# Kernel optimization log

Hardware: AMD Instinct MI355X
Metric: run time of the kernel (lower is better)

The kernel has to match this reference:

```python
import jax, jax.numpy as jnp
import numpy as np

D_MODEL = 1024
NUM_HEADS = 16
D_K = D_MODEL // NUM_HEADS


def setup_inputs() -> dict:
    key = jax.random.key(0)
    ks = jax.random.split(key, 11)
    B, S = 2, 2048
    s = 1.0 / np.sqrt(D_MODEL)
    return {
        "q": jax.random.normal(ks[0], (B, S, D_MODEL), jnp.float32),
        "k": jax.random.normal(ks[1], (B, S, D_MODEL), jnp.float32),
        "v": jax.random.normal(ks[2], (B, S, D_MODEL), jnp.float32),
        "w_q": jax.random.normal(ks[3], (D_MODEL, D_MODEL), jnp.float32) * s,
        "b_q": jnp.zeros((D_MODEL,), jnp.float32),
        "w_k": jax.random.normal(ks[4], (D_MODEL, D_MODEL), jnp.float32) * s,
        "b_k": jnp.zeros((D_MODEL,), jnp.float32),
        "w_v": jax.random.normal(ks[5], (D_MODEL, D_MODEL), jnp.float32) * s,
        "b_v": jnp.zeros((D_MODEL,), jnp.float32),
        "w_o": jax.random.normal(ks[6], (D_MODEL, D_MODEL), jnp.float32) * s,
        "b_o": jnp.zeros((D_MODEL,), jnp.float32),
    }


def reference(q, k, v, w_q, b_q, w_k, b_k, w_v, b_v, w_o, b_o):
    B, S, _ = q.shape
    H, Dk = NUM_HEADS, D_K

    def split_heads(x):  # [B,S,D] -> [B,H,S,Dk]
        return x.reshape(B, S, H, Dk).transpose(0, 2, 1, 3)

    # torch nn.Linear: x @ W.T + b
    qh = split_heads(q @ w_q.T + b_q)
    kh = split_heads(k @ w_k.T + b_k)
    vh = split_heads(v @ w_v.T + b_v)

    scale = 1.0 / jnp.sqrt(jnp.asarray(Dk, qh.dtype))
    scores = jnp.einsum("bhsd,bhtd->bhst", qh, kh) * scale  # [B,H,S,S]
    attn = jax.nn.softmax(scores, axis=-1)
    # dropout is identity in eval/deterministic baseline
    out = jnp.einsum("bhst,bhtd->bhsd", attn, vh)  # [B,H,S,Dk]
    out = out.transpose(0, 2, 1, 3).reshape(B, S, H * Dk)
    return out @ w_o.T + b_o
```

## Files before the change

kernel.cpp:

```cpp
#include <hip/hip_runtime.h>
#include <hip/hip_bf16.h>
#include <stdint.h>

typedef unsigned short u16;
typedef __attribute__((ext_vector_type(8))) short short8;
typedef __attribute__((ext_vector_type(8))) __bf16 bf16x8;
typedef __attribute__((ext_vector_type(4))) float f32x4;
typedef __attribute__((ext_vector_type(4))) uint32_t u32x4;

#if defined(__has_builtin)
#if __has_builtin(__builtin_amdgcn_global_load_lds)
#define USE_GLLDS 1
#endif
#endif

__device__ __forceinline__ u16 f2bf(float f) {
  __hip_bfloat16 h = __float2bfloat16(f);
  return __builtin_bit_cast(u16, h);
}

__device__ __forceinline__ f32x4 mfma16(bf16x8 a, bf16x8 b, f32x4 c) {
  return __builtin_amdgcn_mfma_f32_16x16x32_bf16(a, b, c, 0, 0, 0);
}

#ifdef USE_GLLDS
__device__ __forceinline__ void async_cp16(const void* g, void* l) {
  __builtin_amdgcn_global_load_lds(
      (const __attribute__((address_space(1))) void*)g,
      (__attribute__((address_space(3))) void*)l, 16, 0, 0);
}
#endif

__global__ __launch_bounds__(256) void cvt_all(
    const float* __restrict__ q, const float* __restrict__ k,
    const float* __restrict__ v, const float* __restrict__ w0,
    const float* __restrict__ w1, const float* __restrict__ w2,
    const float* __restrict__ w3, u16* __restrict__ dst) {
  size_t i = ((size_t)blockIdx.x * 256 + threadIdx.x) * 8;
  const size_t M1 = 1u << 20;
  const float* s;
  size_t base;
  if (i < 4 * M1) { s = q; base = 0; }
  else if (i < 8 * M1) { s = k; base = 4 * M1; }
  else if (i < 12 * M1) { s = v; base = 8 * M1; }
  else if (i < 13 * M1) { s = w0; base = 12 * M1; }
  else if (i < 14 * M1) { s = w1; base = 13 * M1; }
  else if (i < 15 * M1) { s = w2; base = 14 * M1; }
  else { s = w3; base = 15 * M1; }
  const float4 a = *(const float4*)(s + (i - base));
  const float4 b = *(const float4*)(s + (i - base) + 4);
  short8 r;
  r[0] = (short)f2bf(a.x); r[1] = (short)f2bf(a.y);
  r[2] = (short)f2bf(a.z); r[3] = (short)f2bf(a.w);
  r[4] = (short)f2bf(b.x); r[5] = (short)f2bf(b.y);
  r[6] = (short)f2bf(b.z); r[7] = (short)f2bf(b.w);
  *(short8*)(dst + i) = r;
}

__device__ __forceinline__ void gemm_body(const u16* __restrict__ X,
                                          const u16* __restrict__ W,
                                          const float* __restrict__ bias,
                                          void* __restrict__ outp, int mode) {
  __shared__ u16 Al[128 * 64];
  __shared__ u16 Bl[128 * 64];
  const int tid = threadIdx.x;
  const int wv = tid >> 6, l = tid & 63;
  const int wr = wv >> 1, wc = wv & 1;
  const int m0 = blockIdx.y * 128, n0 = blockIdx.x * 128;
  const int lrow = l & 15, lk = (l >> 4) * 8;

  f32x4 acc[4][4];
#pragma unroll
  for (int i = 0; i < 4; ++i)
#pragma unroll
    for (int j = 0; j < 4; ++j) acc[i][j] = (f32x4){0.f, 0.f, 0.f, 0.f};

  const u16* Asrc = X + (size_t)(m0 + (tid >> 3)) * 1024 + (tid & 7) * 8;
  const u16* Bsrc = W + (size_t)(n0 + (tid >> 3)) * 1024 + (tid & 7) * 8;

  for (int kt = 0; kt < 1024; kt += 64) {
#ifdef USE_GLLDS
#pragma unroll
    for (int p = 0; p < 4; ++p) {
      async_cp16(Asrc + (size_t)p * 32 * 1024 + kt, &Al[p * 2048 + wv * 512]);
      async_cp16(Bsrc + (size_t)p * 32 * 1024 + kt, &Bl[p * 2048 + wv * 512]);
    }
#else
    short8 ar[4], br[4];
#pragma unroll
    for (int p = 0; p < 4; ++p) {
      ar[p] = *(const short8*)(Asrc + (size_t)p * 32 * 1024 + kt);
      br[p] = *(const short8*)(Bsrc + (size_t)p * 32 * 1024 + kt);
    }
#pragma unroll
    for (int p = 0; p < 4; ++p) {
      *(short8*)&Al[p * 2048 + tid * 8] = ar[p];
      *(short8*)&Bl[p * 2048 + tid * 8] = br[p];
    }
#endif
    __syncthreads();
#pragma unroll
    for (int ks = 0; ks < 2; ++ks) {
      bf16x8 af[4], bf[4];
#pragma unroll
      for (int mf = 0; mf < 4; ++mf)
        af[mf] = *(const bf16x8*)&Al[(wr * 64 + mf * 16 + lrow) * 64 + ks * 32 + lk];
#pragma unroll
      for (int nf = 0; nf < 4; ++nf)
        bf[nf] = *(const bf16x8*)&Bl[(wc * 64 + nf * 16 + lrow) * 64 + ks * 32 + lk];
#pragma unroll
      for (int mf = 0; mf < 4; ++mf)
#pragma unroll
        for (int nf = 0; nf < 4; ++nf)
          acc[mf][nf] = mfma16(af[mf], bf[nf], acc[mf][nf]);
    }
    __syncthreads();
  }

  const int rb = (l >> 4) * 4;
#pragma unroll
  for (int mf = 0; mf < 4; ++mf) {
#pragma unroll
    for (int nf = 0; nf < 4; ++nf) {
      const int gn = n0 + wc * 64 + nf * 16 + lrow;
      const float bi = bias[gn];
#pragma unroll
      for (int r = 0; r < 4; ++r) {
        const int gm = m0 + wr * 64 + mf * 16 + rb + r;
        float val = acc[mf][nf][r] + bi;
        const int b = gm >> 11, s = gm & 2047, h = gn >> 6, d = gn & 63;
        if (mode == 3) {
          ((float*)outp)[(size_t)gm * 1024 + gn] = val;
        } else if (mode == 2) {
          ((u16*)outp)[(((size_t)((b * 16 + h) * 64 + d)) << 11) + s] = f2bf(val);
        } else {
          if (mode == 0) val *= 0.125f;
          ((u16*)outp)[(((size_t)((b * 16 + h) * 2048 + s)) << 6) + d] = f2bf(val);
        }
      }
    }
  }
}

__global__ __launch_bounds__(256) void gemm_proj(
    const u16* __restrict__ qb, const u16* __restrict__ wqb,
    const float* __restrict__ b_q, const float* __restrict__ b_k,
    const float* __restrict__ b_v, u16* __restrict__ Qh) {
  const int z = blockIdx.z;
  const float* bias = (z == 0) ? b_q : ((z == 1) ? b_k : b_v);
  gemm_body(qb + ((size_t)z << 22), wqb + ((size_t)z << 20), bias,
            Qh + ((size_t)z << 22), z);
}

__global__ __launch_bounds__(256) void gemm_out(
    const u16* __restrict__ X, const u16* __restrict__ W,
    const float* __restrict__ bias, float* __restrict__ out) {
  gemm_body(X, W, bias, out, 3);
}

__global__ __launch_bounds__(512, 4) void flash_attn2(
    const u16* __restrict__ Qh, const u16* __restrict__ Kh,
    const u16* __restrict__ VT, u16* __restrict__ AO) {
  __shared__ __align__(16) u16 Kbuf[2][4096];
  __shared__ __align__(16) u16 Vbuf[2][4096];
  __shared__ __align__(16) uint32_t Pl[8 * 576];

  const int tid = threadIdx.x;
  const int wv = tid >> 6, l = tid & 63;
  const int q = l & 15, g = l >> 4;
  const int qt = blockIdx.x, bh = blockIdx.y;

  const u16* Qp = Qh + ((size_t)bh * 2048 + qt * 128 + wv * 16) * 64;
  const u16* Kp = Kh + (size_t)bh * 2048 * 64;
  const u16* Vp = VT + (size_t)bh * 64 * 2048;

  bf16x8 qf[2];
  qf[0] = *(const bf16x8*)(Qp + q * 64 + g * 8);
  qf[1] = *(const bf16x8*)(Qp + q * 64 + 32 + g * 8);

  f32x4 o[4];
#pragma unroll
  for (int df = 0; df < 4; ++df) o[df] = (f32x4){0.f, 0.f, 0.f, 0.f};
  float m = -1e30f, ls = 0.f;

  const int srow = l >> 3;
  const int scolq = (l & 7) ^ srow;
  const int pbase = wv * 576 + q * 36;
  const char* kb0 = (const char*)&Kbuf[0][0];
  const char* kb1 = (const char*)&Kbuf[1][0];
  const char* vb0 = (const char*)&Vbuf[0][0];
  const char* vb1 = (const char*)&Vbuf[1][0];
  const int rsw = (q & 7) << 4;

#ifdef USE_GLLDS
#define STAGE(buf, t)                                                         \
  do {                                                                        \
    const int n0_ = (t) * 64;                                                 \
    const u16* kg_ = Kp + (size_t)(n0_ + wv * 8 + srow) * 64 + scolq * 8;     \
    const u16* vg_ = Vp + (size_t)(wv * 8 + srow) * 2048 + n0_ + scolq * 8;   \
    async_cp16(kg_, &Kbuf[buf][wv * 512]);                                    \
    async_cp16(vg_, &Vbuf[buf][wv * 512]);                                    \
  } while (0)
#else
#define STAGE(buf, t)                                                         \
  do {                                                                        \
    const int n0_ = (t) * 64;                                                 \
    const u16* kg_ = Kp + (size_t)(n0_ + wv * 8 + srow) * 64 + scolq * 8;     \
    const u16* vg_ = Vp + (size_t)(wv * 8 + srow) * 2048 + n0_ + scolq * 8;   \
    short8 kt_ = *(const short8*)kg_;                                         \
    short8 vt_ = *(const short8*)vg_;                                         \
    *(short8*)&Kbuf[buf][wv * 512 + l * 8] = kt_;                             \
    *(short8*)&Vbuf[buf][wv * 512 + l * 8] = vt_;                             \
  } while (0)
#endif

  STAGE(0, 0);
  __syncthreads();

  for (int t = 0; t < 32; ++t) {
    const int cur = t & 1;
    if (t < 31) STAGE(cur ^ 1, t + 1);

    const char* kb = cur ? kb1 : kb0;
    const char* vb = cur ? vb1 : vb0;

    f32x4 s[4];
#pragma unroll
    for (int nj = 0; nj < 4; ++nj) s[nj] = (f32x4){0.f, 0.f, 0.f, 0.f};
#pragma unroll
    for (int ks = 0; ks < 2; ++ks) {
#pragma unroll
      for (int nj = 0; nj < 4; ++nj) {
        bf16x8 kf = *(const bf16x8*)(kb + (nj * 16 + q) * 128 +
                                     (((ks * 4 + g) << 4) ^ rsw));
        s[nj] = mfma16(kf, qf[ks], s[nj]);
      }
    }

    float mt = s[0][0];
#pragma unroll
    for (int nj = 0; nj < 4; ++nj)
#pragma unroll
      for (int r = 0; r < 4; ++r) mt = fmaxf(mt, s[nj][r]);
    mt = fmaxf(mt, __shfl_xor(mt, 16));
    mt = fmaxf(mt, __shfl_xor(mt, 32));
    const float nm = fmaxf(m, mt);
    const float rf = __expf(m - nm);
    m = nm;
    float ps = 0.f;
#pragma unroll
    for (int nj = 0; nj < 4; ++nj)
#pragma unroll
      for (int r = 0; r < 4; ++r) {
        s[nj][r] = __expf(s[nj][r] - nm);
        ps += s[nj][r];
      }
    ps += __shfl_xor(ps, 16);
    ps += __shfl_xor(ps, 32);
    ls = ls * rf + ps;
#pragma unroll
    for (int df = 0; df < 4; ++df) o[df] *= rf;

#pragma unroll
    for (int nj = 0; nj < 4; ++nj)
#pragma unroll
      for (int pp = 0; pp < 2; ++pp) {
        uint32_t w = (uint32_t)f2bf(s[nj][2 * pp]) |
                     ((uint32_t)f2bf(s[nj][2 * pp + 1]) << 16);
        Pl[pbase + nj * 8 + g * 2 + pp] = w;
      }

#pragma unroll
    for (int ks = 0; ks < 2; ++ks) {
      u32x4 pw = *(const u32x4*)&Pl[pbase + ks * 16 + 4 * g];
      bf16x8 pf = __builtin_bit_cast(bf16x8, pw);
#pragma unroll
      for (int df = 0; df < 4; ++df) {
        bf16x8 vf = *(const bf16x8*)(vb + (df * 16 + q) * 128 +
                                     (((ks * 4 + g) << 4) ^ rsw));
        o[df] = mfma16(vf, pf, o[df]);
      }
    }
    __syncthreads();
  }

  const float inv = 1.f / ls;
  const int b = bh >> 4, h = bh & 15;
  u16* Ap = AO + ((size_t)(b * 2048 + qt * 128 + wv * 16 + q)) * 1024 + h * 64;
#pragma unroll
  for (int df = 0; df < 4; ++df)
#pragma unroll
    for (int pp = 0; pp < 2; ++pp) {
      uint32_t w = (uint32_t)f2bf(o[df][2 * pp] * inv) |
                   ((uint32_t)f2bf(o[df][2 * pp + 1] * inv) << 16);
      *(uint32_t*)(Ap + df * 16 + 4 * g + 2 * pp) = w;
    }
}

extern "C" void kernel_launch(void* const* d_in, const int* in_sizes, int n_in,
                              void* d_out, int out_size, void* d_ws,
                              size_t ws_size, hipStream_t stream) {
  const float* q = (const float*)d_in[0];
  const float* k = (const float*)d_in[1];
  const float* v = (const float*)d_in[2];
  const float* w_q = (const float*)d_in[3];
  const float* b_q = (const float*)d_in[4];
  const float* w_k = (const float*)d_in[5];
  const float* b_k = (const float*)d_in[6];
  const float* w_v = (const float*)d_in[7];
  const float* b_v = (const float*)d_in[8];
  const float* w_o = (const float*)d_in[9];
  const float* b_o = (const float*)d_in[10];

  u16* ws = (u16*)d_ws;
  u16* qb = ws;
  u16* wqb = ws + (12u << 20);
  u16* wob = ws + (15u << 20);
  u16* Qh = ws + (16u << 20);
  u16* Kh = ws + (20u << 20);
  u16* VT = ws + (24u << 20);
  u16* AO = ws + (28u << 20);

  cvt_all<<<dim3(8192), dim3(256), 0, stream>>>(q, k, v, w_q, w_k, w_v, w_o, ws);
  gemm_proj<<<dim3(8, 32, 3), dim3(256), 0, stream>>>(qb, wqb, b_q, b_k, b_v, Qh);
  flash_attn2<<<dim3(16, 32), dim3(512), 0, stream>>>(Qh, Kh, VT, AO);
  gemm_out<<<dim3(8, 32), dim3(256), 0, stream>>>(AO, wob, b_o, (float*)d_out);
}
```

Measured before the change: 169.0 us.

## Split attention over KV halves with combine kernel and exp2 lazy rescaling

```diff
diff --git a/kernel.cpp b/kernel.cpp
--- a/kernel.cpp
+++ b/kernel.cpp
@@ -13,6 +13,19 @@
 #define USE_GLLDS 1
 #endif
 #endif
+
+#if defined(__has_builtin)
+#if __has_builtin(__builtin_amdgcn_exp2f)
+#define HAVE_EXP2_BUILTIN 1
+#endif
+#endif
+__device__ __forceinline__ float fexp2(float x) {
+#ifdef HAVE_EXP2_BUILTIN
+  return __builtin_amdgcn_exp2f(x);
+#else
+  return exp2f(x);
+#endif
+}
 
 __device__ __forceinline__ u16 f2bf(float f) {
   __hip_bfloat16 h = __float2bfloat16(f);
@@ -134,7 +147,7 @@
         } else if (mode == 2) {
           ((u16*)outp)[(((size_t)((b * 16 + h) * 64 + d)) << 11) + s] = f2bf(val);
         } else {
-          if (mode == 0) val *= 0.125f;
+          if (mode == 0) val *= 0.18033688f;
           ((u16*)outp)[(((size_t)((b * 16 + h) * 2048 + s)) << 6) + d] = f2bf(val);
         }
       }
@@ -158,17 +171,18 @@
   gemm_body(X, W, bias, out, 3);
 }
 
-__global__ __launch_bounds__(512, 4) void flash_attn2(
+__global__ __launch_bounds__(512, 4) void flash_attn3(
     const u16* __restrict__ Qh, const u16* __restrict__ Kh,
-    const u16* __restrict__ VT, u16* __restrict__ AO) {
-  __shared__ __align__(16) u16 Kbuf[2][4096];
-  __shared__ __align__(16) u16 Vbuf[2][4096];
+    const u16* __restrict__ VT, u16* __restrict__ Op,
+    float2* __restrict__ ml) {
+  __shared__ __align__(16) u16 Kbuf[4096];
+  __shared__ __align__(16) u16 Vbuf[4096];
   __shared__ __align__(16) uint32_t Pl[8 * 576];
 
   const int tid = threadIdx.x;
   const int wv = tid >> 6, l = tid & 63;
   const int q = l & 15, g = l >> 4;
-  const int qt = blockIdx.x, bh = blockIdx.y;
+  const int qt = blockIdx.x, bh = blockIdx.y, z = blockIdx.z;
 
   const u16* Qp = Qh + ((size_t)bh * 2048 + qt * 128 + wv * 16) * 64;
   const u16* Kp = Kh + (size_t)bh * 2048 * 64;
@@ -186,43 +200,36 @@
   const int srow = l >> 3;
   const int scolq = (l & 7) ^ srow;
   const int pbase = wv * 576 + q * 36;
-  const char* kb0 = (const char*)&Kbuf[0][0];
-  const char* kb1 = (const char*)&Kbuf[1][0];
-  const char* vb0 = (const char*)&Vbuf[0][0];
-  const char* vb1 = (const char*)&Vbuf[1][0];
+  const char* kb = (const char*)&Kbuf[0];
+  const char* vb = (const char*)&Vbuf[0];
   const int rsw = (q & 7) << 4;
 
 #ifdef USE_GLLDS
-#define STAGE(buf, t)                                                         \
+#define STAGE(t)                                                              \
   do {                                                                        \
     const int n0_ = (t) * 64;                                                 \
     const u16* kg_ = Kp + (size_t)(n0_ + wv * 8 + srow) * 64 + scolq * 8;     \
     const u16* vg_ = Vp + (size_t)(wv * 8 + srow) * 2048 + n0_ + scolq * 8;   \
-    async_cp16(kg_, &Kbuf[buf][wv * 512]);                                    \
-    async_cp16(vg_, &Vbuf[buf][wv * 512]);                                    \
+    async_cp16(kg_, &Kbuf[wv * 512]);                                         \
+    async_cp16(vg_, &Vbuf[wv * 512]);                                         \
   } while (0)
 #else
-#define STAGE(buf, t)                                                         \
+#define STAGE(t)                                                              \
   do {                                                                        \
     const int n0_ = (t) * 64;                                                 \
     const u16* kg_ = Kp + (size_t)(n0_ + wv * 8 + srow) * 64 + scolq * 8;     \
     const u16* vg_ = Vp + (size_t)(wv * 8 + srow) * 2048 + n0_ + scolq * 8;   \
     short8 kt_ = *(const short8*)kg_;                                         \
     short8 vt_ = *(const short8*)vg_;                                         \
-    *(short8*)&Kbuf[buf][wv * 512 + l * 8] = kt_;                             \
-    *(short8*)&Vbuf[buf][wv * 512 + l * 8] = vt_;                             \
+    *(short8*)&Kbuf[wv * 512 + l * 8] = kt_;                                  \
+    *(short8*)&Vbuf[wv * 512 + l * 8] = vt_;                                  \
   } while (0)
 #endif
 
-  STAGE(0, 0);
-  __syncthreads();
-
-  for (int t = 0; t < 32; ++t) {
-    const int cur = t & 1;
-    if (t < 31) STAGE(cur ^ 1, t + 1);
-
-    const char* kb = cur ? kb1 : kb0;
-    const char* vb = cur ? vb1 : vb0;
+  const int t0 = z * 16;
+  for (int tt = 0; tt < 16; ++tt) {
+    STAGE(t0 + tt);
+    __syncthreads();
 
     f32x4 s[4];
 #pragma unroll
@@ -237,29 +244,32 @@
       }
     }
 
-    float mt = s[0][0];
-#pragma unroll
-    for (int nj = 0; nj < 4; ++nj)
-#pragma unroll
-      for (int r = 0; r < 4; ++r) mt = fmaxf(mt, s[nj][r]);
+    const float a0 = fmaxf(fmaxf(s[0][0], s[0][1]), fmaxf(s[0][2], s[0][3]));
+    const float a1 = fmaxf(fmaxf(s[1][0], s[1][1]), fmaxf(s[1][2], s[1][3]));
+    const float a2 = fmaxf(fmaxf(s[2][0], s[2][1]), fmaxf(s[2][2], s[2][3]));
+    const float a3 = fmaxf(fmaxf(s[3][0], s[3][1]), fmaxf(s[3][2], s[3][3]));
+    float mt = fmaxf(fmaxf(a0, a1), fmaxf(a2, a3));
     mt = fmaxf(mt, __shfl_xor(mt, 16));
     mt = fmaxf(mt, __shfl_xor(mt, 32));
-    const float nm = fmaxf(m, mt);
-    const float rf = __expf(m - nm);
-    m = nm;
+    if (!__all(mt <= m + 8.f)) {
+      const float nm = fmaxf(m, mt);
+      const float rf = fexp2(m - nm);
+      m = nm;
+      ls *= rf;
+#pragma unroll
+      for (int df = 0; df < 4; ++df) o[df] *= rf;
+    }
     float ps = 0.f;
 #pragma unroll
     for (int nj = 0; nj < 4; ++nj)
 #pragma unroll
       for (int r = 0; r < 4; ++r) {
-        s[nj][r] = __expf(s[nj][r] - nm);
+        s[nj][r] = fexp2(s[nj][r] - m);
         ps += s[nj][r];
       }
     ps += __shfl_xor(ps, 16);
     ps += __shfl_xor(ps, 32);
-    ls = ls * rf + ps;
-#pragma unroll
-    for (int df = 0; df < 4; ++df) o[df] *= rf;
+    ls += ps;
 
 #pragma unroll
     for (int nj = 0; nj < 4; ++nj)
@@ -285,16 +295,42 @@
   }
 
   const float inv = 1.f / ls;
-  const int b = bh >> 4, h = bh & 15;
-  u16* Ap = AO + ((size_t)(b * 2048 + qt * 128 + wv * 16 + q)) * 1024 + h * 64;
+  const int rowb = qt * 128 + wv * 16 + q;
+  const size_t prow = (size_t)(z * 32 + bh) * 2048 + rowb;
+  u16* Po = Op + (prow << 6);
 #pragma unroll
   for (int df = 0; df < 4; ++df)
 #pragma unroll
     for (int pp = 0; pp < 2; ++pp) {
       uint32_t w = (uint32_t)f2bf(o[df][2 * pp] * inv) |
                    ((uint32_t)f2bf(o[df][2 * pp + 1] * inv) << 16);
-      *(uint32_t*)(Ap + df * 16 + 4 * g + 2 * pp) = w;
-    }
+      *(uint32_t*)(Po + df * 16 + 4 * g + 2 * pp) = w;
+    }
+  if (g == 0) ml[prow] = make_float2(m, ls);
+}
+
+__global__ __launch_bounds__(256) void combine(
+    const uint32_t* __restrict__ Op32, const float2* __restrict__ ml,
+    u16* __restrict__ AO) {
+  const int j = blockIdx.x * 256 + threadIdx.x;
+  const int rowid = j >> 5, w5 = j & 31;
+  const float2 a = ml[rowid];
+  const float2 c = ml[(1 << 16) + rowid];
+  const float M = fmaxf(a.x, c.x);
+  float w1 = a.y * fexp2(a.x - M);
+  float w2 = c.y * fexp2(c.x - M);
+  const float inv = 1.f / (w1 + w2);
+  w1 *= inv;
+  w2 *= inv;
+  const uint32_t p1 = Op32[j];
+  const uint32_t p2 = Op32[(1u << 21) + j];
+  const float lo = w1 * __builtin_bit_cast(float, p1 << 16) +
+                   w2 * __builtin_bit_cast(float, p2 << 16);
+  const float hi = w1 * __builtin_bit_cast(float, p1 & 0xffff0000u) +
+                   w2 * __builtin_bit_cast(float, p2 & 0xffff0000u);
+  const uint32_t outw = (uint32_t)f2bf(lo) | ((uint32_t)f2bf(hi) << 16);
+  const int bh = rowid >> 11, s = rowid & 2047, b = bh >> 4, h = bh & 15;
+  ((uint32_t*)AO)[((size_t)(b * 2048 + s) << 9) + h * 32 + w5] = outw;
 }
 
 extern "C" void kernel_launch(void* const* d_in, const int* in_sizes, int n_in,
@@ -320,9 +356,12 @@
   u16* Kh = ws + (20u << 20);
   u16* VT = ws + (24u << 20);
   u16* AO = ws + (28u << 20);
+  u16* Op = ws;
+  float2* ml = (float2*)(ws + (8u << 20));
 
   cvt_all<<<dim3(8192), dim3(256), 0, stream>>>(q, k, v, w_q, w_k, w_v, w_o, ws);
   gemm_proj<<<dim3(8, 32, 3), dim3(256), 0, stream>>>(qb, wqb, b_q, b_k, b_v, Qh);
-  flash_attn2<<<dim3(16, 32), dim3(512), 0, stream>>>(Qh, Kh, VT, AO);
+  flash_attn3<<<dim3(16, 32, 2), dim3(512), 0, stream>>>(Qh, Kh, VT, Op, ml);
+  combine<<<dim3(8192), dim3(256), 0, stream>>>((const uint32_t*)Op, ml, AO);
   gemm_out<<<dim3(8, 32), dim3(256), 0, stream>>>(AO, wob, b_o, (float*)d_out);
 }
```

Result: slower. 173.9 us (+2.9%).
